# Kernel tuning notes

Hardware: AMD Instinct MI355X
Metric: run time of the kernel (lower is better)

## Reference

```python
import jax, jax.numpy as jnp
import numpy as np

NUM_VALUES = 32
NUM_DUPES = 4
M = NUM_VALUES * NUM_DUPES  # num_values_with_dupes = 128
N = 131072                  # batch of evaluation points
SMOOTHING_WIDTH = 0.1
USE_ARGMAX = False          # forward default


def setup_inputs() -> dict:
    key = jax.random.key(0)
    kx, ks, kl, kr = jax.random.split(key, 4)
    x = jax.random.uniform(kx, (N,), dtype=jnp.float32)  # points in [0, 1]
    # torch.rand(M)*0.5 + 0.25
    split_points_param = jax.random.uniform(ks, (M,), dtype=jnp.float32) * 0.5 + 0.25
    # torch.linspace(0, 1, num_values)
    values_param = jnp.linspace(0.0, 1.0, NUM_VALUES, dtype=jnp.float32)
    # one-hot random row matrices (requires_grad=False in the original)
    li = jax.random.randint(kl, (M,), 0, M)
    ri = jax.random.randint(kr, (M,), 0, M)
    left_matrix = jnp.zeros((M, M), jnp.float32).at[jnp.arange(M), li].set(1.0)
    right_matrix = jnp.zeros((M, M), jnp.float32).at[jnp.arange(M), ri].set(1.0)
    return {
        "x": x,
        "split_points_param": split_points_param,
        "values_param": values_param,
        "left_matrix": left_matrix,
        "right_matrix": right_matrix,
        "max_depth": 10,
    }


def _fractal_forward(x, split_points_param, values_param, left_matrix, right_matrix,
                     max_depth, use_argmax):
    # property transforms from the module
    split_points = jax.nn.sigmoid(split_points_param * 4.0 - 2.0)      # [M]
    values = jnp.tile(values_param * 3.0 + 1.0, NUM_DUPES)             # [M]
    n = x.shape[0]
    m = split_points.shape[0]
    # soft distribution over fractal nodes, start at root node 0
    w = jnp.zeros((n, m), x.dtype).at[:, 0].set(1.0)                   # [N, M]
    lo = jnp.zeros_like(x)
    hi = jnp.ones_like(x)
    for _ in range(max_depth):
        # split location inside the current interval of each point
        s = lo + (w @ split_points) * (hi - lo)                         # [N]
        if use_argmax:
            t = (x >= s).astype(x.dtype)
        else:
            t = jax.nn.sigmoid((x - s) / SMOOTHING_WIDTH)               # [N]
        # descend: blend left/right child node distributions
        w = (1.0 - t)[:, None] * (w @ left_matrix) + t[:, None] * (w @ right_matrix)
        # contract intervals toward the chosen side
        lo, hi = (1.0 - t) * lo + t * s, (1.0 - t) * s + t * hi
    return w @ values                                                   # [N]


def reference(x, split_points_param, values_param, left_matrix, right_matrix, max_depth):
    return _fractal_forward(x, split_points_param, values_param,
                            left_matrix, right_matrix, int(max_depth), USE_ARGMAX)
```

## Files before the change

### kernel.cpp

```cpp
#include <hip/hip_runtime.h>

#define M 128
#define BT 64

typedef _Float16 half8 __attribute__((ext_vector_type(8)));
typedef __fp16 fp16x2 __attribute__((ext_vector_type(2)));
typedef float f32x4 __attribute__((ext_vector_type(4)));


__global__ void setup_kernel(const float* __restrict__ spp,
                             const float* __restrict__ vp,
                             const float* __restrict__ Lm,
                             const float* __restrict__ Rm,
                             float* __restrict__ ws) {
  __shared__ float ssp[M], svl[M];
  __shared__ int sli[M], sri[M];
  __shared__ float sT[1024];
  __shared__ float sV10[1024];
  __shared__ int cur[1024], nxt[1024];
  const int t = threadIdx.x;
  if (t < M) {
    ssp[t] = 1.f / (1.f + __expf(2.f - 4.f * spp[t]));
    svl[t] = vp[t & 31] * 3.f + 1.f;
  }
  {
    const int row = t & (M - 1);
    const float* Mt = (t < M) ? Lm : Rm;
    const float4* r4 = (const float4*)(Mt + row * M);
    int idx = 0;
#pragma unroll
    for (int j4 = 0; j4 < M / 4; ++j4) {
      const float4 v = r4[j4];
      if (v.x > 0.5f) idx = 4 * j4;
      if (v.y > 0.5f) idx = 4 * j4 + 1;
      if (v.z > 0.5f) idx = 4 * j4 + 2;
      if (v.w > 0.5f) idx = 4 * j4 + 3;
    }
    if (t < M) sli[row] = idx; else sri[row] = idx;
  }
  if (t == 0) { cur[0] = 0; sT[0] = 0.f; }
  __syncthreads();
  if (t < M) {
    ws[3072 + t] = ssp[t];
    ws[3200 + t] = svl[t];
    ((int*)ws)[3328 + t] = sli[t];
    ((int*)ws)[3456 + t] = sri[t];
  }
  int S = 1;
  for (int d = 0; d <= 10; ++d) {
    for (int i = t; i < S; i += 256) {
      const int nd = cur[i];
      if (d <= 9) sT[S + i] = ssp[nd];
      else sV10[i] = svl[nd];
      if (d < 10) { nxt[2 * i] = sli[nd]; nxt[2 * i + 1] = sri[nd]; }
    }
    __syncthreads();
    if (d < 10) {
      for (int i = t; i < 2 * S; i += 256) cur[i] = nxt[i];
      __syncthreads();
    }
    S <<= 1;
  }
  unsigned* fbout = (unsigned*)(ws + 4096);
  for (int d = t; d < 1024; d += 256) {
    const int dw = d & 3;
    const int lane = (d >> 2) & 63;
    const int rt = d >> 9;
    const int ks = (d >> 8) & 1;
    const int m = lane & 15, gg = lane >> 4;
    const int prow = rt * 16 + m;
    float v[2];
#pragma unroll
    for (int h = 0; h < 2; ++h) {
      const int e = 2 * dw + h;
      const int kl = (e < 4) ? (4 * gg + e) : (16 + 4 * gg + (e - 4));
      const int i = ks * 32 + kl;
      float val;
      if (prow == 0) val = sT[64 + i];
      else if (prow < 3) val = sT[128 + 2 * i + (prow - 1)];
      else if (prow < 7) val = sT[256 + 4 * i + (prow - 3)];
      else if (prow < 15) val = sT[512 + 8 * i + (prow - 7)];
      else if (prow < 31) val = sV10[16 * i + (prow - 15)];
      else val = 0.f;
      v[h] = val;
    }
    union { fp16x2 h; unsigned u; } pu;
    pu.h = __builtin_amdgcn_cvt_pkrtz(v[0], v[1]);
    fbout[d] = pu.u;
  }
  if (t < 64) ws[t] = sT[t];
}

#define PSTEP(S)                                                              \
  {                                                                           \
    float dot = 0.f;                                                          \
    _Pragma("unroll") for (int i = 0; i < (S); ++i)                           \
        dot = fmaf(c[i], sT[(S) + i], dot);                                   \
    const float sv = fmaf(dot, hi - lo, lo);                                  \
    tt = 1.f / (1.f + __expf((sv - xv) * 10.f));                              \
    uu = 1.f - tt;                                                            \
    const float nlo = fmaf(tt, sv, uu * lo);                                  \
    const float nhi = fmaf(tt, hi, uu * sv);                                  \
    lo = nlo; hi = nhi;                                                       \
    _Pragma("unroll") for (int i = (S)-1; i >= 0; --i) {                      \
      const float v = c[i];                                                   \
      c[2 * i + 1] = v * tt;                                                  \
      c[2 * i] = v * uu;                                                      \
    }                                                                         \
  }

#define SIGSTEP(dotv)                                   \
  {                                                     \
    const float sv = fmaf((dotv), hi - lo, lo);         \
    tt = 1.f / (1.f + __expf((sv - xv) * 10.f));        \
    uu = 1.f - tt;                                      \
    const float nlo = fmaf(tt, sv, uu * lo);            \
    const float nhi = fmaf(tt, hi, uu * sv);            \
    lo = nlo; hi = nhi;                                 \
  }

__launch_bounds__(BT)
__global__ void fractal10(const float* __restrict__ x,
                          const int* __restrict__ dpt,
                          float* __restrict__ out, int n,
                          const float* __restrict__ ws) {
  if (dpt[0] != 10) return;
  __shared__ float sT[64];
  __shared__ __align__(16) float sbuf[64 * 32];
  const int l = threadIdx.x;
  const int gid = blockIdx.x * BT + l;

  sT[l] = ws[l];
  const float4* fb = (const float4*)(ws + 4096);
  union f4h8 { float4 f; half8 h; };
  f4h8 A00, A01, A10, A11;
  A00.f = fb[0 * 64 + l];
  A01.f = fb[1 * 64 + l];
  A10.f = fb[2 * 64 + l];
  A11.f = fb[3 * 64 + l];
  const float xv = (gid < n) ? x[gid] : 0.5f;
  __syncthreads();

  float c[64];
  float lo = 0.f, hi = 1.f, tt, uu;
  c[0] = 1.f;
  PSTEP(1) PSTEP(2) PSTEP(4) PSTEP(8) PSTEP(16) PSTEP(32)

  {
    char* cb = (char*)sbuf + l * 128;
#pragma unroll
    for (int q = 0; q < 8; ++q) {
      const int k0 = (q >> 2) * 32 + (q & 3) * 4;
      union { fp16x2 h2[4]; float4 f4; } u;
      u.h2[0] = __builtin_amdgcn_cvt_pkrtz(c[k0], c[k0 + 1]);
      u.h2[1] = __builtin_amdgcn_cvt_pkrtz(c[k0 + 2], c[k0 + 3]);
      u.h2[2] = __builtin_amdgcn_cvt_pkrtz(c[k0 + 16], c[k0 + 17]);
      u.h2[3] = __builtin_amdgcn_cvt_pkrtz(c[k0 + 18], c[k0 + 19]);
      *(float4*)(cb + ((q ^ (l & 7)) * 16)) = u.f4;
    }
  }
  __syncthreads();

  half8 bf[2][4];
  const int col = l & 15, g = l >> 4;
#pragma unroll
  for (int ct = 0; ct < 4; ++ct) {
    const int p = 16 * ct + col;
    const char* pb = (const char*)sbuf + p * 128;
#pragma unroll
    for (int ks = 0; ks < 2; ++ks) {
      const int q = ks * 4 + g;
      bf[ks][ct] = *(const half8*)(pb + ((q ^ (p & 7)) * 16));
    }
  }
  __syncthreads();

  f32x4 acc[2][4];
#pragma unroll
  for (int rt = 0; rt < 2; ++rt)
#pragma unroll
    for (int ct = 0; ct < 4; ++ct) acc[rt][ct] = f32x4{0.f, 0.f, 0.f, 0.f};
#pragma unroll
  for (int ct = 0; ct < 4; ++ct) {
    acc[0][ct] = __builtin_amdgcn_mfma_f32_16x16x32_f16(A00.h, bf[0][ct], acc[0][ct], 0, 0, 0);
    acc[0][ct] = __builtin_amdgcn_mfma_f32_16x16x32_f16(A01.h, bf[1][ct], acc[0][ct], 0, 0, 0);
    acc[1][ct] = __builtin_amdgcn_mfma_f32_16x16x32_f16(A10.h, bf[0][ct], acc[1][ct], 0, 0, 0);
    acc[1][ct] = __builtin_amdgcn_mfma_f32_16x16x32_f16(A11.h, bf[1][ct], acc[1][ct], 0, 0, 0);
  }

#pragma unroll
  for (int rt = 0; rt < 2; ++rt)
#pragma unroll
    for (int ct = 0; ct < 4; ++ct) {
      const int p = 16 * ct + col;
      const int rb = rt * 4 + g;
      *(f32x4*)((char*)sbuf + p * 128 + ((rb ^ (p & 7)) * 16)) = acc[rt][ct];
    }
  __syncthreads();
  float4 P[8];
#pragma unroll
  for (int j = 0; j < 8; ++j)
    P[j] = *(const float4*)((const char*)sbuf + l * 128 + ((j ^ (l & 7)) * 16));

  SIGSTEP(P[0].x);
  const float w20 = uu, w21 = tt;
  SIGSTEP(fmaf(w20, P[0].y, w21 * P[0].z));
  float W4[4] = {w20 * uu, w20 * tt, w21 * uu, w21 * tt};
  SIGSTEP(fmaf(W4[0], P[0].w, fmaf(W4[1], P[1].x, fmaf(W4[2], P[1].y, W4[3] * P[1].z))));
  float W8[8];
#pragma unroll
  for (int s = 3; s >= 0; --s) { W8[2 * s + 1] = W4[s] * tt; W8[2 * s] = W4[s] * uu; }
  {
    float d0 = fmaf(W8[0], P[1].w, W8[1] * P[2].x);
    float d1 = fmaf(W8[2], P[2].y, W8[3] * P[2].z);
    float d2 = fmaf(W8[4], P[2].w, W8[5] * P[3].x);
    float d3 = fmaf(W8[6], P[3].y, W8[7] * P[3].z);
    SIGSTEP((d0 + d1) + (d2 + d3));
  }
  float W16[16];
#pragma unroll
  for (int s = 7; s >= 0; --s) { W16[2 * s + 1] = W8[s] * tt; W16[2 * s] = W8[s] * uu; }
  float outv;
  {
    float d0 = fmaf(W16[0], P[3].w, W16[1] * P[4].x);
    d0 = fmaf(W16[2], P[4].y, d0); d0 = fmaf(W16[3], P[4].z, d0);
    float d1 = fmaf(W16[4], P[4].w, W16[5] * P[5].x);
    d1 = fmaf(W16[6], P[5].y, d1); d1 = fmaf(W16[7], P[5].z, d1);
    float d2 = fmaf(W16[8], P[5].w, W16[9] * P[6].x);
    d2 = fmaf(W16[10], P[6].y, d2); d2 = fmaf(W16[11], P[6].z, d2);
    float d3 = fmaf(W16[12], P[6].w, W16[13] * P[7].x);
    d3 = fmaf(W16[14], P[7].y, d3); d3 = fmaf(W16[15], P[7].z, d3);
    outv = (d0 + d1) + (d2 + d3);
  }
  if (gid < n) out[gid] = outv;
}

__launch_bounds__(64)
__global__ void fractal_generic(const float* __restrict__ x,
                                const int* __restrict__ dpt,
                                float* __restrict__ out, int n,
                                const float* __restrict__ ws) {
  const int depth = dpt[0];
  if (depth == 10) return;
  __shared__ float w[2][M][64];
  const int t = threadIdx.x;
  const float* sp = ws + 3072;
  const float* vals = ws + 3200;
  const int* li = (const int*)ws + 3328;
  const int* ri = (const int*)ws + 3456;
  for (int gid = blockIdx.x * 64 + t; gid < n; gid += gridDim.x * 64) {
    const float xv = x[gid];
    for (int j = 0; j < M; ++j) w[0][j][t] = 0.f;
    w[0][0][t] = 1.f;
    float lo = 0.f, hi = 1.f;
    int cb = 0;
    for (int k = 0; k < depth; ++k) {
      float dot = 0.f;
      for (int j = 0; j < M; ++j) dot += w[cb][j][t] * sp[j];
      const float sv = lo + dot * (hi - lo);
      const float tt = 1.f / (1.f + __expf((sv - xv) * 10.f));
      const float uu = 1.f - tt;
      for (int j = 0; j < M; ++j) w[cb ^ 1][j][t] = 0.f;
      for (int j = 0; j < M; ++j) {
        const float v = w[cb][j][t];
        w[cb ^ 1][li[j]][t] += uu * v;
        w[cb ^ 1][ri[j]][t] += tt * v;
      }
      const float nlo = uu * lo + tt * sv;
      const float nhi = uu * sv + tt * hi;
      lo = nlo; hi = nhi;
      cb ^= 1;
    }
    float acc = 0.f;
    for (int j = 0; j < M; ++j) acc += w[cb][j][t] * vals[j];
    out[gid] = acc;
  }
}

extern "C" void kernel_launch(void* const* d_in, const int* in_sizes, int n_in,
                              void* d_out, int out_size, void* d_ws, size_t ws_size,
                              hipStream_t stream) {
  const float* x   = (const float*)d_in[0];
  const float* spp = (const float*)d_in[1];
  const float* vp  = (const float*)d_in[2];
  const float* Lm  = (const float*)d_in[3];
  const float* Rm  = (const float*)d_in[4];
  const int* dpt   = (const int*)d_in[5];
  float* out = (float*)d_out;
  float* ws = (float*)d_ws;
  const int n = in_sizes[0];

  hipLaunchKernelGGL(setup_kernel, dim3(1), dim3(256), 0, stream, spp, vp, Lm, Rm, ws);
  const int blocks = (n + BT - 1) / BT;
  hipLaunchKernelGGL(fractal10, dim3(blocks), dim3(BT), 0, stream,
                     x, dpt, out, n, (const float*)ws);
  hipLaunchKernelGGL(fractal_generic, dim3(128), dim3(64), 0, stream, x, dpt, out, n,
                     (const float*)ws);
}
```

Baseline: 19.73 us.

## Fuse setup, depth-10 and generic kernels into one launch with 256-thread blocks

```diff
diff --git a/kernel.cpp b/kernel.cpp
--- a/kernel.cpp
+++ b/kernel.cpp
@@ -1,94 +1,53 @@
 #include <hip/hip_runtime.h>
 
 #define M 128
-#define BT 64
+#define BT 256
 
 typedef _Float16 half8 __attribute__((ext_vector_type(8)));
 typedef __fp16 fp16x2 __attribute__((ext_vector_type(2)));
 typedef float f32x4 __attribute__((ext_vector_type(4)));
 
-
-__global__ void setup_kernel(const float* __restrict__ spp,
-                             const float* __restrict__ vp,
-                             const float* __restrict__ Lm,
-                             const float* __restrict__ Rm,
-                             float* __restrict__ ws) {
-  __shared__ float ssp[M], svl[M];
-  __shared__ int sli[M], sri[M];
-  __shared__ float sT[1024];
-  __shared__ float sV10[1024];
-  __shared__ int cur[1024], nxt[1024];
-  const int t = threadIdx.x;
-  if (t < M) {
-    ssp[t] = 1.f / (1.f + __expf(2.f - 4.f * spp[t]));
-    svl[t] = vp[t & 31] * 3.f + 1.f;
-  }
-  {
-    const int row = t & (M - 1);
-    const float* Mt = (t < M) ? Lm : Rm;
-    const float4* r4 = (const float4*)(Mt + row * M);
-    int idx = 0;
-#pragma unroll
-    for (int j4 = 0; j4 < M / 4; ++j4) {
-      const float4 v = r4[j4];
-      if (v.x > 0.5f) idx = 4 * j4;
-      if (v.y > 0.5f) idx = 4 * j4 + 1;
-      if (v.z > 0.5f) idx = 4 * j4 + 2;
-      if (v.w > 0.5f) idx = 4 * j4 + 3;
-    }
-    if (t < M) sli[row] = idx; else sri[row] = idx;
-  }
-  if (t == 0) { cur[0] = 0; sT[0] = 0.f; }
-  __syncthreads();
-  if (t < M) {
-    ws[3072 + t] = ssp[t];
-    ws[3200 + t] = svl[t];
-    ((int*)ws)[3328 + t] = sli[t];
-    ((int*)ws)[3456 + t] = sri[t];
-  }
-  int S = 1;
-  for (int d = 0; d <= 10; ++d) {
-    for (int i = t; i < S; i += 256) {
-      const int nd = cur[i];
-      if (d <= 9) sT[S + i] = ssp[nd];
-      else sV10[i] = svl[nd];
-      if (d < 10) { nxt[2 * i] = sli[nd]; nxt[2 * i + 1] = sri[nd]; }
-    }
-    __syncthreads();
-    if (d < 10) {
-      for (int i = t; i < 2 * S; i += 256) cur[i] = nxt[i];
-      __syncthreads();
-    }
-    S <<= 1;
-  }
-  unsigned* fbout = (unsigned*)(ws + 4096);
-  for (int d = t; d < 1024; d += 256) {
-    const int dw = d & 3;
-    const int lane = (d >> 2) & 63;
-    const int rt = d >> 9;
-    const int ks = (d >> 8) & 1;
-    const int m = lane & 15, gg = lane >> 4;
-    const int prow = rt * 16 + m;
+struct FastMem {
+  float sT[1024];
+  float sV10[1024];
+  int cur[1024];
+  int nxt[1024];
+  float4 sbuf[256 * 8];
+};
+union SMem {
+  FastMem f;
+  float wfb[2][M][64];
+};
+
+__device__ __forceinline__ float tb_gather(const float* sT, const float* sV10,
+                                           int prow, int i) {
+  if (prow == 0) return sT[64 + i];
+  if (prow < 3) return sT[128 + 2 * i + (prow - 1)];
+  if (prow < 7) return sT[256 + 4 * i + (prow - 3)];
+  if (prow < 15) return sT[512 + 8 * i + (prow - 7)];
+  if (prow < 31) return sV10[16 * i + (prow - 15)];
+  return 0.f;
+}
+
+__device__ __forceinline__ half8 build_frag(const float* sT, const float* sV10,
+                                            int rt, int ks, int m, int gg) {
+  union { unsigned u[4]; half8 h; } r;
+  const int prow = rt * 16 + m;
+#pragma unroll
+  for (int dw = 0; dw < 4; ++dw) {
     float v[2];
 #pragma unroll
     for (int h = 0; h < 2; ++h) {
       const int e = 2 * dw + h;
       const int kl = (e < 4) ? (4 * gg + e) : (16 + 4 * gg + (e - 4));
       const int i = ks * 32 + kl;
-      float val;
-      if (prow == 0) val = sT[64 + i];
-      else if (prow < 3) val = sT[128 + 2 * i + (prow - 1)];
-      else if (prow < 7) val = sT[256 + 4 * i + (prow - 3)];
-      else if (prow < 15) val = sT[512 + 8 * i + (prow - 7)];
-      else if (prow < 31) val = sV10[16 * i + (prow - 15)];
-      else val = 0.f;
-      v[h] = val;
-    }
-    union { fp16x2 h; unsigned u; } pu;
-    pu.h = __builtin_amdgcn_cvt_pkrtz(v[0], v[1]);
-    fbout[d] = pu.u;
-  }
-  if (t < 64) ws[t] = sT[t];
+      v[h] = tb_gather(sT, sV10, prow, i);
+    }
+    union { fp16x2 p; unsigned u; } pu;
+    pu.p = __builtin_amdgcn_cvt_pkrtz(v[0], v[1]);
+    r.u[dw] = pu.u;
+  }
+  return r.h;
 }
 
 #define PSTEP(S)                                                              \
@@ -120,160 +79,197 @@
   }
 
 __launch_bounds__(BT)
-__global__ void fractal10(const float* __restrict__ x,
-                          const int* __restrict__ dpt,
-                          float* __restrict__ out, int n,
-                          const float* __restrict__ ws) {
-  if (dpt[0] != 10) return;
-  __shared__ float sT[64];
-  __shared__ __align__(16) float sbuf[64 * 32];
-  const int l = threadIdx.x;
-  const int gid = blockIdx.x * BT + l;
-
-  sT[l] = ws[l];
-  const float4* fb = (const float4*)(ws + 4096);
-  union f4h8 { float4 f; half8 h; };
-  f4h8 A00, A01, A10, A11;
-  A00.f = fb[0 * 64 + l];
-  A01.f = fb[1 * 64 + l];
-  A10.f = fb[2 * 64 + l];
-  A11.f = fb[3 * 64 + l];
-  const float xv = (gid < n) ? x[gid] : 0.5f;
+__global__ void fractal_fused(const float* __restrict__ x,
+                              const float* __restrict__ spp,
+                              const float* __restrict__ vp,
+                              const float* __restrict__ Lm,
+                              const float* __restrict__ Rm,
+                              const int* __restrict__ dpt,
+                              float* __restrict__ out, int n) {
+  __shared__ float ssp[M], svl[M];
+  __shared__ int sli[M], sri[M];
+  __shared__ SMem U;
+  const int t = threadIdx.x;
+  const int depth = dpt[0];
+
+  if (t < M) {
+    ssp[t] = 1.f / (1.f + __expf(2.f - 4.f * spp[t]));
+    svl[t] = vp[t & 31] * 3.f + 1.f;
+  }
+  {
+    const int row = t & (M - 1);
+    const float* Mt = (t < M) ? Lm : Rm;
+    const float4* r4 = (const float4*)(Mt + row * M);
+    int idx = 0;
+#pragma unroll
+    for (int j4 = 0; j4 < M / 4; ++j4) {
+      const float4 v = r4[j4];
+      if (v.x > 0.5f) idx = 4 * j4;
+      if (v.y > 0.5f) idx = 4 * j4 + 1;
+      if (v.z > 0.5f) idx = 4 * j4 + 2;
+      if (v.w > 0.5f) idx = 4 * j4 + 3;
+    }
+    if (t < M) sli[row] = idx; else sri[row] = idx;
+  }
   __syncthreads();
 
-  float c[64];
-  float lo = 0.f, hi = 1.f, tt, uu;
-  c[0] = 1.f;
-  PSTEP(1) PSTEP(2) PSTEP(4) PSTEP(8) PSTEP(16) PSTEP(32)
-
-  {
-    char* cb = (char*)sbuf + l * 128;
-#pragma unroll
-    for (int q = 0; q < 8; ++q) {
-      const int k0 = (q >> 2) * 32 + (q & 3) * 4;
-      union { fp16x2 h2[4]; float4 f4; } u;
-      u.h2[0] = __builtin_amdgcn_cvt_pkrtz(c[k0], c[k0 + 1]);
-      u.h2[1] = __builtin_amdgcn_cvt_pkrtz(c[k0 + 2], c[k0 + 3]);
-      u.h2[2] = __builtin_amdgcn_cvt_pkrtz(c[k0 + 16], c[k0 + 17]);
-      u.h2[3] = __builtin_amdgcn_cvt_pkrtz(c[k0 + 18], c[k0 + 19]);
-      *(float4*)(cb + ((q ^ (l & 7)) * 16)) = u.f4;
-    }
-  }
-  __syncthreads();
-
-  half8 bf[2][4];
-  const int col = l & 15, g = l >> 4;
-#pragma unroll
-  for (int ct = 0; ct < 4; ++ct) {
-    const int p = 16 * ct + col;
-    const char* pb = (const char*)sbuf + p * 128;
-#pragma unroll
-    for (int ks = 0; ks < 2; ++ks) {
-      const int q = ks * 4 + g;
-      bf[ks][ct] = *(const half8*)(pb + ((q ^ (p & 7)) * 16));
-    }
-  }
-  __syncthreads();
-
-  f32x4 acc[2][4];
-#pragma unroll
-  for (int rt = 0; rt < 2; ++rt)
-#pragma unroll
-    for (int ct = 0; ct < 4; ++ct) acc[rt][ct] = f32x4{0.f, 0.f, 0.f, 0.f};
-#pragma unroll
-  for (int ct = 0; ct < 4; ++ct) {
-    acc[0][ct] = __builtin_amdgcn_mfma_f32_16x16x32_f16(A00.h, bf[0][ct], acc[0][ct], 0, 0, 0);
-    acc[0][ct] = __builtin_amdgcn_mfma_f32_16x16x32_f16(A01.h, bf[1][ct], acc[0][ct], 0, 0, 0);
-    acc[1][ct] = __builtin_amdgcn_mfma_f32_16x16x32_f16(A10.h, bf[0][ct], acc[1][ct], 0, 0, 0);
-    acc[1][ct] = __builtin_amdgcn_mfma_f32_16x16x32_f16(A11.h, bf[1][ct], acc[1][ct], 0, 0, 0);
-  }
-
-#pragma unroll
-  for (int rt = 0; rt < 2; ++rt)
+  if (depth == 10) {
+    float* sT = U.f.sT;
+    float* sV10 = U.f.sV10;
+    if (t == 0) { U.f.cur[0] = 0; sT[0] = 0.f; }
+    __syncthreads();
+    int S = 1;
+    for (int d = 0; d <= 10; ++d) {
+      for (int i = t; i < S; i += BT) {
+        const int nd = U.f.cur[i];
+        if (d <= 9) sT[S + i] = ssp[nd];
+        else sV10[i] = svl[nd];
+        if (d < 10) { U.f.nxt[2 * i] = sli[nd]; U.f.nxt[2 * i + 1] = sri[nd]; }
+      }
+      __syncthreads();
+      if (d < 10) {
+        for (int i = t; i < 2 * S; i += BT) U.f.cur[i] = U.f.nxt[i];
+        __syncthreads();
+      }
+      S <<= 1;
+    }
+
+    const int lane = t & 63;
+    const int col = lane & 15, g = lane >> 4;
+    const half8 A00 = build_frag(sT, sV10, 0, 0, col, g);
+    const half8 A01 = build_frag(sT, sV10, 0, 1, col, g);
+    const half8 A10 = build_frag(sT, sV10, 1, 0, col, g);
+    const half8 A11 = build_frag(sT, sV10, 1, 1, col, g);
+
+    const int gid = blockIdx.x * BT + t;
+    const float xv = (gid < n) ? x[gid] : 0.5f;
+
+    float c[64];
+    float lo = 0.f, hi = 1.f, tt, uu;
+    c[0] = 1.f;
+    PSTEP(1) PSTEP(2) PSTEP(4) PSTEP(8) PSTEP(16) PSTEP(32)
+
+    char* const sb = (char*)U.f.sbuf;
+    {
+      char* cb = sb + t * 128;
+#pragma unroll
+      for (int q = 0; q < 8; ++q) {
+        const int k0 = (q >> 2) * 32 + (q & 3) * 4;
+        union { fp16x2 h2[4]; float4 f4; } u;
+        u.h2[0] = __builtin_amdgcn_cvt_pkrtz(c[k0], c[k0 + 1]);
+        u.h2[1] = __builtin_amdgcn_cvt_pkrtz(c[k0 + 2], c[k0 + 3]);
+        u.h2[2] = __builtin_amdgcn_cvt_pkrtz(c[k0 + 16], c[k0 + 17]);
+        u.h2[3] = __builtin_amdgcn_cvt_pkrtz(c[k0 + 18], c[k0 + 19]);
+        *(float4*)(cb + ((q ^ (t & 7)) * 16)) = u.f4;
+      }
+    }
+    __syncthreads();
+
+    const int wbase = (t >> 6) << 6;
+    half8 bf[2][4];
 #pragma unroll
     for (int ct = 0; ct < 4; ++ct) {
-      const int p = 16 * ct + col;
-      const int rb = rt * 4 + g;
-      *(f32x4*)((char*)sbuf + p * 128 + ((rb ^ (p & 7)) * 16)) = acc[rt][ct];
-    }
-  __syncthreads();
-  float4 P[8];
-#pragma unroll
-  for (int j = 0; j < 8; ++j)
-    P[j] = *(const float4*)((const char*)sbuf + l * 128 + ((j ^ (l & 7)) * 16));
-
-  SIGSTEP(P[0].x);
-  const float w20 = uu, w21 = tt;
-  SIGSTEP(fmaf(w20, P[0].y, w21 * P[0].z));
-  float W4[4] = {w20 * uu, w20 * tt, w21 * uu, w21 * tt};
-  SIGSTEP(fmaf(W4[0], P[0].w, fmaf(W4[1], P[1].x, fmaf(W4[2], P[1].y, W4[3] * P[1].z))));
-  float W8[8];
-#pragma unroll
-  for (int s = 3; s >= 0; --s) { W8[2 * s + 1] = W4[s] * tt; W8[2 * s] = W4[s] * uu; }
-  {
-    float d0 = fmaf(W8[0], P[1].w, W8[1] * P[2].x);
-    float d1 = fmaf(W8[2], P[2].y, W8[3] * P[2].z);
-    float d2 = fmaf(W8[4], P[2].w, W8[5] * P[3].x);
-    float d3 = fmaf(W8[6], P[3].y, W8[7] * P[3].z);
-    SIGSTEP((d0 + d1) + (d2 + d3));
-  }
-  float W16[16];
-#pragma unroll
-  for (int s = 7; s >= 0; --s) { W16[2 * s + 1] = W8[s] * tt; W16[2 * s] = W8[s] * uu; }
-  float outv;
-  {
-    float d0 = fmaf(W16[0], P[3].w, W16[1] * P[4].x);
-    d0 = fmaf(W16[2], P[4].y, d0); d0 = fmaf(W16[3], P[4].z, d0);
-    float d1 = fmaf(W16[4], P[4].w, W16[5] * P[5].x);
-    d1 = fmaf(W16[6], P[5].y, d1); d1 = fmaf(W16[7], P[5].z, d1);
-    float d2 = fmaf(W16[8], P[5].w, W16[9] * P[6].x);
-    d2 = fmaf(W16[10], P[6].y, d2); d2 = fmaf(W16[11], P[6].z, d2);
-    float d3 = fmaf(W16[12], P[6].w, W16[13] * P[7].x);
-    d3 = fmaf(W16[14], P[7].y, d3); d3 = fmaf(W16[15], P[7].z, d3);
-    outv = (d0 + d1) + (d2 + d3);
-  }
-  if (gid < n) out[gid] = outv;
-}
-
-__launch_bounds__(64)
-__global__ void fractal_generic(const float* __restrict__ x,
-                                const int* __restrict__ dpt,
-                                float* __restrict__ out, int n,
-                                const float* __restrict__ ws) {
-  const int depth = dpt[0];
-  if (depth == 10) return;
-  __shared__ float w[2][M][64];
-  const int t = threadIdx.x;
-  const float* sp = ws + 3072;
-  const float* vals = ws + 3200;
-  const int* li = (const int*)ws + 3328;
-  const int* ri = (const int*)ws + 3456;
-  for (int gid = blockIdx.x * 64 + t; gid < n; gid += gridDim.x * 64) {
-    const float xv = x[gid];
-    for (int j = 0; j < M; ++j) w[0][j][t] = 0.f;
-    w[0][0][t] = 1.f;
-    float lo = 0.f, hi = 1.f;
-    int cb = 0;
-    for (int k = 0; k < depth; ++k) {
-      float dot = 0.f;
-      for (int j = 0; j < M; ++j) dot += w[cb][j][t] * sp[j];
-      const float sv = lo + dot * (hi - lo);
-      const float tt = 1.f / (1.f + __expf((sv - xv) * 10.f));
-      const float uu = 1.f - tt;
-      for (int j = 0; j < M; ++j) w[cb ^ 1][j][t] = 0.f;
-      for (int j = 0; j < M; ++j) {
-        const float v = w[cb][j][t];
-        w[cb ^ 1][li[j]][t] += uu * v;
-        w[cb ^ 1][ri[j]][t] += tt * v;
-      }
-      const float nlo = uu * lo + tt * sv;
-      const float nhi = uu * sv + tt * hi;
-      lo = nlo; hi = nhi;
-      cb ^= 1;
-    }
-    float acc = 0.f;
-    for (int j = 0; j < M; ++j) acc += w[cb][j][t] * vals[j];
-    out[gid] = acc;
+      const int p = wbase + 16 * ct + col;
+      const char* pb = sb + p * 128;
+#pragma unroll
+      for (int ks = 0; ks < 2; ++ks) {
+        const int q = ks * 4 + g;
+        bf[ks][ct] = *(const half8*)(pb + ((q ^ (p & 7)) * 16));
+      }
+    }
+    __syncthreads();
+
+    f32x4 acc[2][4];
+#pragma unroll
+    for (int rt = 0; rt < 2; ++rt)
+#pragma unroll
+      for (int ct = 0; ct < 4; ++ct) acc[rt][ct] = f32x4{0.f, 0.f, 0.f, 0.f};
+#pragma unroll
+    for (int ct = 0; ct < 4; ++ct) {
+      acc[0][ct] = __builtin_amdgcn_mfma_f32_16x16x32_f16(A00, bf[0][ct], acc[0][ct], 0, 0, 0);
+      acc[0][ct] = __builtin_amdgcn_mfma_f32_16x16x32_f16(A01, bf[1][ct], acc[0][ct], 0, 0, 0);
+      acc[1][ct] = __builtin_amdgcn_mfma_f32_16x16x32_f16(A10, bf[0][ct], acc[1][ct], 0, 0, 0);
+      acc[1][ct] = __builtin_amdgcn_mfma_f32_16x16x32_f16(A11, bf[1][ct], acc[1][ct], 0, 0, 0);
+    }
+
+#pragma unroll
+    for (int rt = 0; rt < 2; ++rt)
+#pragma unroll
+      for (int ct = 0; ct < 4; ++ct) {
+        const int p = wbase + 16 * ct + col;
+        const int rb = rt * 4 + g;
+        *(f32x4*)(sb + p * 128 + ((rb ^ (p & 7)) * 16)) = acc[rt][ct];
+      }
+    __syncthreads();
+    float4 P[8];
+#pragma unroll
+    for (int j = 0; j < 8; ++j)
+      P[j] = *(const float4*)(sb + t * 128 + ((j ^ (t & 7)) * 16));
+
+    SIGSTEP(P[0].x);
+    const float w20 = uu, w21 = tt;
+    SIGSTEP(fmaf(w20, P[0].y, w21 * P[0].z));
+    float W4[4] = {w20 * uu, w20 * tt, w21 * uu, w21 * tt};
+    SIGSTEP(fmaf(W4[0], P[0].w, fmaf(W4[1], P[1].x, fmaf(W4[2], P[1].y, W4[3] * P[1].z))));
+    float W8[8];
+#pragma unroll
+    for (int s = 3; s >= 0; --s) { W8[2 * s + 1] = W4[s] * tt; W8[2 * s] = W4[s] * uu; }
+    {
+      float d0 = fmaf(W8[0], P[1].w, W8[1] * P[2].x);
+      float d1 = fmaf(W8[2], P[2].y, W8[3] * P[2].z);
+      float d2 = fmaf(W8[4], P[2].w, W8[5] * P[3].x);
+      float d3 = fmaf(W8[6], P[3].y, W8[7] * P[3].z);
+      SIGSTEP((d0 + d1) + (d2 + d3));
+    }
+    float W16[16];
+#pragma unroll
+    for (int s = 7; s >= 0; --s) { W16[2 * s + 1] = W8[s] * tt; W16[2 * s] = W8[s] * uu; }
+    float outv;
+    {
+      float d0 = fmaf(W16[0], P[3].w, W16[1] * P[4].x);
+      d0 = fmaf(W16[2], P[4].y, d0); d0 = fmaf(W16[3], P[4].z, d0);
+      float d1 = fmaf(W16[4], P[4].w, W16[5] * P[5].x);
+      d1 = fmaf(W16[6], P[5].y, d1); d1 = fmaf(W16[7], P[5].z, d1);
+      float d2 = fmaf(W16[8], P[5].w, W16[9] * P[6].x);
+      d2 = fmaf(W16[10], P[6].y, d2); d2 = fmaf(W16[11], P[6].z, d2);
+      float d3 = fmaf(W16[12], P[6].w, W16[13] * P[7].x);
+      d3 = fmaf(W16[14], P[7].y, d3); d3 = fmaf(W16[15], P[7].z, d3);
+      outv = (d0 + d1) + (d2 + d3);
+    }
+    if (gid < n) out[gid] = outv;
+  } else {
+    for (int base = blockIdx.x * 64; base < n; base += gridDim.x * 64) {
+      if (t < 64) {
+        const int gid = base + t;
+        if (gid < n) {
+          const float xv = x[gid];
+          for (int j = 0; j < M; ++j) U.wfb[0][j][t] = 0.f;
+          U.wfb[0][0][t] = 1.f;
+          float lo = 0.f, hi = 1.f;
+          int cb = 0;
+          for (int k = 0; k < depth; ++k) {
+            float dot = 0.f;
+            for (int j = 0; j < M; ++j) dot += U.wfb[cb][j][t] * ssp[j];
+            const float sv = lo + dot * (hi - lo);
+            const float tt2 = 1.f / (1.f + __expf((sv - xv) * 10.f));
+            const float uu2 = 1.f - tt2;
+            for (int j = 0; j < M; ++j) U.wfb[cb ^ 1][j][t] = 0.f;
+            for (int j = 0; j < M; ++j) {
+              const float v = U.wfb[cb][j][t];
+              U.wfb[cb ^ 1][sli[j]][t] += uu2 * v;
+              U.wfb[cb ^ 1][sri[j]][t] += tt2 * v;
+            }
+            const float nlo = uu2 * lo + tt2 * sv;
+            const float nhi = uu2 * sv + tt2 * hi;
+            lo = nlo; hi = nhi;
+            cb ^= 1;
+          }
+          float acc = 0.f;
+          for (int j = 0; j < M; ++j) acc += U.wfb[cb][j][t] * svl[j];
+          out[gid] = acc;
+        }
+      }
+    }
   }
 }
 
@@ -287,13 +283,9 @@
   const float* Rm  = (const float*)d_in[4];
   const int* dpt   = (const int*)d_in[5];
   float* out = (float*)d_out;
-  float* ws = (float*)d_ws;
   const int n = in_sizes[0];
 
-  hipLaunchKernelGGL(setup_kernel, dim3(1), dim3(256), 0, stream, spp, vp, Lm, Rm, ws);
   const int blocks = (n + BT - 1) / BT;
-  hipLaunchKernelGGL(fractal10, dim3(blocks), dim3(BT), 0, stream,
-                     x, dpt, out, n, (const float*)ws);
-  hipLaunchKernelGGL(fractal_generic, dim3(128), dim3(64), 0, stream, x, dpt, out, n,
-                     (const float*)ws);
-}
+  hipLaunchKernelGGL(fractal_fused, dim3(blocks), dim3(BT), 0, stream,
+                     x, spp, vp, Lm, Rm, dpt, out, n);
+}
```

New measurement: 19.76 us. About the same (+0.1%).
